# Performance work log

Measured on AMD Instinct MI355X. Metric: run time of the kernel, lower is better.

The kernel has to match this reference:

```python
import jax, jax.numpy as jnp
import numpy as np

N, D = 16384, 256

def setup_inputs() -> dict:
    key = jax.random.key(0)
    k1, k2, k3 = jax.random.split(key, 3)
    X = jax.random.normal(k1, (N, D), dtype=jnp.float32)
    W = jax.random.normal(k2, (D, D), dtype=jnp.float32) * (1.0 / np.sqrt(D))
    b = jax.random.normal(k3, (D,), dtype=jnp.float32) * (1.0 / np.sqrt(D))
    return {"X": X, "W": W, "b": b}

def reference(X, W, b):
    # Step 1: bilinear attention A = X W X^T   (N, N) -- materialized as in original
    A = (X @ W) @ X.T
    # Step 2: context aggregation Z = A X      (N, D)
    Z = A @ X
    # Step 3: output head g = Z b              (N,)
    g = Z @ b
    return g
```

## Files before the change

kernel.cpp:

```cpp
#include <hip/hip_runtime.h>

#define NROWS 16384
#define DDIM  256
#define GBLK  2048
#define NSLOT 64


#define SUB1  0
#define MAIN1 2048
#define GO1   2080
#define SUB2  4128
#define MAIN2 6176
#define GO2   6208
#define REFC  8256

__device__ __forceinline__ unsigned aload(const unsigned* p) {
    return __hip_atomic_load(p, __ATOMIC_RELAXED, __HIP_MEMORY_SCOPE_AGENT);
}
__device__ __forceinline__ float afload(const float* p) {
    return __hip_atomic_load(p, __ATOMIC_RELAXED, __HIP_MEMORY_SCOPE_AGENT);
}

__device__ __forceinline__ void gbar(unsigned* __restrict__ bars, int sub,
                                     int mn, int go, unsigned initv) {
    asm volatile("s_waitcnt vmcnt(0)" ::: "memory");
    __syncthreads();
    if (threadIdx.x == 0) {
        const int grp = blockIdx.x >> 5;
        const int mem = blockIdx.x & 31;
        unsigned old = __hip_atomic_fetch_add(&bars[sub + grp * 32], 1u,
                          __ATOMIC_RELAXED, __HIP_MEMORY_SCOPE_AGENT);
        if (old - initv == 31u)
            __hip_atomic_fetch_add(&bars[mn], 1u,
                __ATOMIC_RELAXED, __HIP_MEMORY_SCOPE_AGENT);
        unsigned spins = 0;
        if (mem == 0) {
            while (aload(&bars[mn]) - initv < 64u) {
                __builtin_amdgcn_s_sleep(8);
                if (++spins > 200000u) break;
            }
            __hip_atomic_store(&bars[go + grp * 32], initv + 1u,
                __ATOMIC_RELAXED, __HIP_MEMORY_SCOPE_AGENT);
        } else {
            while (aload(&bars[go + grp * 32]) - initv == 0u) {
                __builtin_amdgcn_s_sleep(8);
                if (++spins > 200000u) break;
            }
        }
    }
    __syncthreads();
}

__global__ __launch_bounds__(256, 8)
void fused(const float* __restrict__ X, const float* __restrict__ W,
           const float* __restrict__ b, float* __restrict__ slots,
           float* __restrict__ w2, unsigned* __restrict__ bars,
           float* __restrict__ g) {
    const int tid  = threadIdx.x;
    const int lane = tid & 63;
    const int wave = tid >> 6;
    const int bid  = blockIdx.x;

    __shared__ __align__(16) float sp[4][DDIM];
    __shared__ __align__(16) float sv[DDIM];

    const float4* X4 = (const float4*)X;

    unsigned initv = 0;
    if (tid == 0) initv = aload(&bars[REFC]);

    {
        const float4 bf = ((const float4*)b)[lane];
        float4 vacc = make_float4(0.f, 0.f, 0.f, 0.f);
        const int row0 = bid * 8 + wave * 2;
        #pragma unroll
        for (int i = 0; i < 2; ++i) {
            const float4 xv = X4[(row0 + i) * 64 + lane];
            float t = xv.x * bf.x + xv.y * bf.y + xv.z * bf.z + xv.w * bf.w;
            #pragma unroll
            for (int off = 32; off; off >>= 1) t += __shfl_xor(t, off, 64);
            vacc.x += t * xv.x; vacc.y += t * xv.y;
            vacc.z += t * xv.z; vacc.w += t * xv.w;
        }
        ((float4*)sp[wave])[lane] = vacc;
        __syncthreads();
        const float s = sp[0][tid] + sp[1][tid] + sp[2][tid] + sp[3][tid];
        atomicAdd(&slots[(bid & (NSLOT - 1)) * DDIM + tid], s);
    }

    gbar(bars, SUB1, MAIN1, GO1, initv);

    if (bid < NSLOT) {
        float acc = 0.f;
        #pragma unroll 8
        for (int r = 0; r < NSLOT; ++r)
            acc += afload(&slots[r * DDIM + tid]);
        sv[tid] = acc;
        __syncthreads();
        const float4 vf = ((const float4*)sv)[lane];
        const int row = bid * 4 + wave;
        const float4 w = ((const float4*)W)[row * 64 + lane];
        float t = w.x * vf.x + w.y * vf.y + w.z * vf.z + w.w * vf.w;
        #pragma unroll
        for (int off = 32; off; off >>= 1) t += __shfl_xor(t, off, 64);
        if (lane == 0)
            __hip_atomic_store(&w2[row], t, __ATOMIC_RELAXED,
                               __HIP_MEMORY_SCOPE_AGENT);
    }

    gbar(bars, SUB2, MAIN2, GO2, initv);

    {
        sv[tid] = afload(&w2[tid]);
        __syncthreads();
        const float4 wf = ((const float4*)sv)[lane];
        const int row0 = bid * 8 + wave * 2;
        #pragma unroll
        for (int i = 0; i < 2; ++i) {
            const float4 xv = X4[(row0 + i) * 64 + lane];
            float t = xv.x * wf.x + xv.y * wf.y + xv.z * wf.z + xv.w * wf.w;
            #pragma unroll
            for (int off = 32; off; off >>= 1) t += __shfl_xor(t, off, 64);
            if (lane == 0) g[row0 + i] = t;
        }
    }
}

extern "C" void kernel_launch(void* const* d_in, const int* in_sizes, int n_in,
                              void* d_out, int out_size, void* d_ws, size_t ws_size,
                              hipStream_t stream) {
    const float* X = (const float*)d_in[0];
    const float* W = (const float*)d_in[1];
    const float* b = (const float*)d_in[2];
    float* g = (float*)d_out;

    float*    slots = (float*)d_ws;
    float*    w2    = slots + NSLOT * DDIM;
    unsigned* bars  = (unsigned*)d_ws + 32768;

    fused<<<GBLK, 256, 0, stream>>>(X, W, b, slots, w2, bars, g);
}
```

Baseline: 76.62 us.

## Replace slot atomics with per-block partials and simplify the second grid barrier

Each block now writes its b-weighted partial sum to its own row of a workspace buffer, with plain stores instead of contended atomicAdds into 64 slots. After the first barrier, 8 blocks each reduce 32 columns across all 2048 partials and atomically add their slice of the W product into w2, which is zeroed earlier in the kernel. The second barrier then waits only on those 8 producer blocks instead of a full grid arrive. In exchange, the cross-grid reduction is concentrated in 8 blocks doing long strided load chains, which may lengthen the critical path.

```diff
diff --git a/kernel.cpp b/kernel.cpp
--- a/kernel.cpp
+++ b/kernel.cpp
@@ -3,16 +3,15 @@
 #define NROWS 16384
 #define DDIM  256
 #define GBLK  2048
-#define NSLOT 64
+#define PBLK  8
 
 
 #define SUB1  0
 #define MAIN1 2048
 #define GO1   2080
-#define SUB2  4128
-#define MAIN2 6176
-#define GO2   6208
-#define REFC  8256
+#define MAIN2 4128
+#define GO2   4160
+#define REFC  6208
 
 __device__ __forceinline__ unsigned aload(const unsigned* p) {
     return __hip_atomic_load(p, __ATOMIC_RELAXED, __HIP_MEMORY_SCOPE_AGENT);
@@ -20,40 +19,16 @@
 __device__ __forceinline__ float afload(const float* p) {
     return __hip_atomic_load(p, __ATOMIC_RELAXED, __HIP_MEMORY_SCOPE_AGENT);
 }
-
-__device__ __forceinline__ void gbar(unsigned* __restrict__ bars, int sub,
-                                     int mn, int go, unsigned initv) {
-    asm volatile("s_waitcnt vmcnt(0)" ::: "memory");
-    __syncthreads();
-    if (threadIdx.x == 0) {
-        const int grp = blockIdx.x >> 5;
-        const int mem = blockIdx.x & 31;
-        unsigned old = __hip_atomic_fetch_add(&bars[sub + grp * 32], 1u,
-                          __ATOMIC_RELAXED, __HIP_MEMORY_SCOPE_AGENT);
-        if (old - initv == 31u)
-            __hip_atomic_fetch_add(&bars[mn], 1u,
-                __ATOMIC_RELAXED, __HIP_MEMORY_SCOPE_AGENT);
-        unsigned spins = 0;
-        if (mem == 0) {
-            while (aload(&bars[mn]) - initv < 64u) {
-                __builtin_amdgcn_s_sleep(8);
-                if (++spins > 200000u) break;
-            }
-            __hip_atomic_store(&bars[go + grp * 32], initv + 1u,
-                __ATOMIC_RELAXED, __HIP_MEMORY_SCOPE_AGENT);
-        } else {
-            while (aload(&bars[go + grp * 32]) - initv == 0u) {
-                __builtin_amdgcn_s_sleep(8);
-                if (++spins > 200000u) break;
-            }
-        }
-    }
-    __syncthreads();
+__device__ __forceinline__ void astore(float* p, float v) {
+    __hip_atomic_store(p, v, __ATOMIC_RELAXED, __HIP_MEMORY_SCOPE_AGENT);
+}
+__device__ __forceinline__ unsigned armw(unsigned* p) {
+    return __hip_atomic_fetch_add(p, 1u, __ATOMIC_RELAXED, __HIP_MEMORY_SCOPE_AGENT);
 }
 
 __global__ __launch_bounds__(256, 8)
 void fused(const float* __restrict__ X, const float* __restrict__ W,
-           const float* __restrict__ b, float* __restrict__ slots,
+           const float* __restrict__ b, float* __restrict__ p1,
            float* __restrict__ w2, unsigned* __restrict__ bars,
            float* __restrict__ g) {
     const int tid  = threadIdx.x;
@@ -61,7 +36,7 @@
     const int wave = tid >> 6;
     const int bid  = blockIdx.x;
 
-    __shared__ __align__(16) float sp[4][DDIM];
+    __shared__ __align__(16) float sp[4 * DDIM];
     __shared__ __align__(16) float sv[DDIM];
 
     const float4* X4 = (const float4*)X;
@@ -82,33 +57,94 @@
             vacc.x += t * xv.x; vacc.y += t * xv.y;
             vacc.z += t * xv.z; vacc.w += t * xv.w;
         }
-        ((float4*)sp[wave])[lane] = vacc;
+        ((float4*)&sp[wave * DDIM])[lane] = vacc;
         __syncthreads();
-        const float s = sp[0][tid] + sp[1][tid] + sp[2][tid] + sp[3][tid];
-        atomicAdd(&slots[(bid & (NSLOT - 1)) * DDIM + tid], s);
+        const float s = sp[tid] + sp[DDIM + tid] + sp[2*DDIM + tid] + sp[3*DDIM + tid];
+        astore(&p1[bid * DDIM + tid], s);
+        if (bid == GBLK - 1) astore(&w2[tid], 0.f);
     }
 
-    gbar(bars, SUB1, MAIN1, GO1, initv);
+    asm volatile("s_waitcnt vmcnt(0)" ::: "memory");
+    __syncthreads();
+    if (tid == 0) {
+        const int grp = bid >> 5, mem = bid & 31;
+        unsigned old = armw(&bars[SUB1 + grp * 32]);
+        if (old - initv == 31u) armw(&bars[MAIN1]);
+        unsigned spins = 0;
+        if (mem == 0) {
+            while (aload(&bars[MAIN1]) - initv < 64u) {
+                __builtin_amdgcn_s_sleep(4);
+                if (++spins > 400000u) break;
+            }
+            __hip_atomic_store(&bars[GO1 + grp * 32], initv + 1u,
+                               __ATOMIC_RELAXED, __HIP_MEMORY_SCOPE_AGENT);
+        } else {
+            while (aload(&bars[GO1 + grp * 32]) - initv == 0u) {
+                __builtin_amdgcn_s_sleep(4);
+                if (++spins > 400000u) break;
+            }
+        }
+    }
+    __syncthreads();
 
-    if (bid < NSLOT) {
+    if (bid < PBLK) {
+        const int c   = tid & 31;
+        const int seg = tid >> 5;
+        const float* base = p1 + (seg * 256) * DDIM + bid * 32 + c;
         float acc = 0.f;
-        #pragma unroll 8
-        for (int r = 0; r < NSLOT; ++r)
-            acc += afload(&slots[r * DDIM + tid]);
-        sv[tid] = acc;
+        for (int it = 0; it < 256; it += 8) {
+            const float t0 = afload(base + (it + 0) * DDIM);
+            const float t1 = afload(base + (it + 1) * DDIM);
+            const float t2 = afload(base + (it + 2) * DDIM);
+            const float t3 = afload(base + (it + 3) * DDIM);
+            const float t4 = afload(base + (it + 4) * DDIM);
+            const float t5 = afload(base + (it + 5) * DDIM);
+            const float t6 = afload(base + (it + 6) * DDIM);
+            const float t7 = afload(base + (it + 7) * DDIM);
+            acc += ((t0 + t1) + (t2 + t3)) + ((t4 + t5) + (t6 + t7));
+        }
+        sp[seg * 32 + c] = acc;
         __syncthreads();
-        const float4 vf = ((const float4*)sv)[lane];
-        const int row = bid * 4 + wave;
-        const float4 w = ((const float4*)W)[row * 64 + lane];
-        float t = w.x * vf.x + w.y * vf.y + w.z * vf.z + w.w * vf.w;
+        if (tid < 32) {
+            float v = 0.f;
+            #pragma unroll
+            for (int s2 = 0; s2 < 8; ++s2) v += sp[s2 * 32 + tid];
+            sv[tid] = v;
+        }
+        __syncthreads();
+        const float4* W4  = (const float4*)W;
+        const float4* sv4 = (const float4*)sv;
+        float w2p = 0.f;
         #pragma unroll
-        for (int off = 32; off; off >>= 1) t += __shfl_xor(t, off, 64);
-        if (lane == 0)
-            __hip_atomic_store(&w2[row], t, __ATOMIC_RELAXED,
-                               __HIP_MEMORY_SCOPE_AGENT);
+        for (int k = 0; k < 8; ++k) {
+            const float4 wv = W4[tid * 64 + bid * 8 + k];
+            const float4 vv = sv4[k];
+            w2p += wv.x * vv.x + wv.y * vv.y + wv.z * vv.z + wv.w * vv.w;
+        }
+        atomicAdd(&w2[tid], w2p);
     }
 
-    gbar(bars, SUB2, MAIN2, GO2, initv);
+    asm volatile("s_waitcnt vmcnt(0)" ::: "memory");
+    __syncthreads();
+    if (tid == 0) {
+        if (bid < PBLK) armw(&bars[MAIN2]);
+        const int grp = bid >> 5, mem = bid & 31;
+        unsigned spins = 0;
+        if (mem == 0) {
+            while (aload(&bars[MAIN2]) - initv < (unsigned)PBLK) {
+                __builtin_amdgcn_s_sleep(4);
+                if (++spins > 400000u) break;
+            }
+            __hip_atomic_store(&bars[GO2 + grp * 32], initv + 1u,
+                               __ATOMIC_RELAXED, __HIP_MEMORY_SCOPE_AGENT);
+        } else {
+            while (aload(&bars[GO2 + grp * 32]) - initv == 0u) {
+                __builtin_amdgcn_s_sleep(4);
+                if (++spins > 400000u) break;
+            }
+        }
+    }
+    __syncthreads();
 
     {
         sv[tid] = afload(&w2[tid]);
@@ -134,9 +170,9 @@
     const float* b = (const float*)d_in[2];
     float* g = (float*)d_out;
 
-    float*    slots = (float*)d_ws;
-    float*    w2    = slots + NSLOT * DDIM;
-    unsigned* bars  = (unsigned*)d_ws + 32768;
+    float*    p1   = (float*)d_ws;
+    float*    w2   = p1 + GBLK * DDIM;
+    unsigned* bars = (unsigned*)d_ws + 532480;
 
-    fused<<<GBLK, 256, 0, stream>>>(X, W, b, slots, w2, bars, g);
+    fused<<<GBLK, 256, 0, stream>>>(X, W, b, p1, w2, bars, g);
 }
```

New measurement: 78.38 us. +2.3%, slower.
